# Optimization experiments

Measured on AMD Instinct MI355X. Metric: run time of the kernel, lower is better.

Reference implementation:

```python
import jax, jax.numpy as jnp
import numpy as np

N_INP = 128
N_HID = 512
N_OUT = 256
N_HEADS = 64
N_SM = 4
EPS_GN = 1e-5
TINY = 1e-14


def setup_inputs() -> dict:
    key = jax.random.key(0)
    ks = jax.random.split(key, 8)
    s = 0.05  # small init scale keeps softplus/softmax in a sane range
    f32 = jnp.float32
    return {
        "x": jax.random.normal(ks[0], (N_INP, N_INP), f32),
        "last_out_sm": jax.random.uniform(ks[1], (N_OUT, N_HEADS), f32),
        # grouped-conv weights, stored per-head with conv singleton dims squeezed
        "qw": jax.random.normal(ks[2], (N_HEADS, N_INP), f32) * s,            # Conv2d q
        "w1": jax.random.normal(ks[3], (N_HEADS, N_HID, N_INP), f32) * s,     # Conv1d l1
        "gn1_g": jnp.ones((N_HEADS, N_HID), f32),                             # GroupNorm ln_l1
        "gn1_b": jnp.zeros((N_HEADS, N_HID), f32),
        "w2": jax.random.normal(ks[4], (N_SM, N_HEADS, N_OUT, N_HID), f32) * s,  # Conv1d l2_n
        "gn2_g": jnp.ones((N_SM, N_HEADS, N_OUT), f32),                       # GroupNorm ln_l2_n
        "gn2_b": jnp.zeros((N_SM, N_HEADS, N_OUT), f32),
        "ws": jax.random.normal(ks[5], (N_HEADS, N_OUT, N_OUT), f32) * s,     # Conv1d scalar
        "woo": jax.random.normal(ks[6], (N_HEADS, 2 * N_OUT), f32) * s,       # Conv1d on_off
    }


def _group_norm(z, g, b):
    # normalize over the last (per-head channel) axis, biased variance, then affine
    mu = z.mean(-1, keepdims=True)
    var = z.var(-1, keepdims=True)
    return (z - mu) * jax.lax.rsqrt(var + EPS_GN) * g + b


def reference(x, last_out_sm, qw, w1, gn1_g, gn1_b, w2, gn2_g, gn2_b, ws, woo):
    n_out = last_out_sm.shape[0]
    # q: grouped Conv2d with kernel (1, n_inp) on replicated x -> per-head x @ qw_h
    sub = jnp.einsum("rc,hc->hr", x, qw)                     # (H, n_inp)
    # l1 (grouped 1x1 conv == per-head matmul) + GroupNorm(n_heads groups) + softplus
    h1 = jax.nn.softplus(_group_norm(jnp.einsum("hoi,hi->ho", w1, sub), gn1_g, gn1_b))  # (H, n_hid)
    # l2_n branches: per-head matmul + GroupNorm + softmax over n_out, summed over n_sm
    z = _group_norm(jnp.einsum("shoi,hi->sho", w2, h1), gn2_g, gn2_b)  # (S, H, n_out)
    out_sm = jax.nn.softmax(z, axis=-1).sum(0).T             # (n_out, H)
    # scalar branch: grouped 1x1 conv applied to ones -> row-sum of per-head weight
    scalar = ws.sum(-1).T                                    # (n_out, H)
    # on_off gate: per-head dot of [prod(last_out_sm, dim1), out_sm[:, h]] with woo_h
    last_prod = jnp.prod(last_out_sm, axis=1)                # (n_out,)
    gate_logit = woo[:, :n_out] @ last_prod + jnp.einsum("ho,oh->h", woo[:, n_out:], out_sm)
    on_off = jax.nn.sigmoid(gate_logit)                      # (H,)
    on_off_out_sm = on_off[None, :] * out_sm                 # (n_out, H)
    out_scaled = on_off_out_sm * scalar
    out_scaled = jnp.where(jnp.abs(out_scaled) <= TINY, TINY, out_scaled)
    return (jnp.clip(on_off_out_sm, TINY, None), out_scaled)
```

## Files before the change

kernel.cpp:

```cpp
#include <hip/hip_runtime.h>
#include <math.h>

#define N_INP 128
#define N_HID 512
#define N_OUT 256
#define N_HEADS 64
#define N_SM 4
#define EPS_GN 1e-5f
#define TINY 1e-14f

__device__ __forceinline__ float wave_sum(float v) {
#pragma unroll
  for (int off = 32; off; off >>= 1) v += __shfl_down(v, off);
  return v;
}
__device__ __forceinline__ float wave_max(float v) {
#pragma unroll
  for (int off = 32; off; off >>= 1) v = fmaxf(v, __shfl_down(v, off));
  return v;
}

__device__ __forceinline__ float block_sum(float v, float* red) {
  int wave = threadIdx.x >> 6, lane = threadIdx.x & 63;
  int nw = blockDim.x >> 6;
  v = wave_sum(v);
  __syncthreads();
  if (lane == 0) red[wave] = v;
  __syncthreads();
  float s = 0.f;
  for (int i = 0; i < nw; ++i) s += red[i];
  return s;
}
__device__ __forceinline__ float block_max(float v, float* red) {
  int wave = threadIdx.x >> 6, lane = threadIdx.x & 63;
  int nw = blockDim.x >> 6;
  v = wave_max(v);
  __syncthreads();
  if (lane == 0) red[wave] = v;
  __syncthreads();
  float s = -3.4e38f;
  for (int i = 0; i < nw; ++i) s = fmaxf(s, red[i]);
  return s;
}

__global__ __launch_bounds__(512) void k_z1(
    const float* __restrict__ x, const float* __restrict__ qw,
    const float* __restrict__ w1, float* __restrict__ z1,
    float* __restrict__ osm) {
  int blk = blockIdx.x;
  int h = blk >> 2, oq = blk & 3;
  int tid = threadIdx.x, wave = tid >> 6, lane = tid & 63;
  __shared__ float sub_s[N_INP];

  if (tid < 64) osm[blk * 64 + tid] = 0.f;

  float2 qv = ((const float2*)(qw + h * N_INP))[lane];
  for (int r = wave; r < N_INP; r += 8) {
    float2 xv = ((const float2*)(x + r * N_INP))[lane];
    float p = wave_sum(xv.x * qv.x + xv.y * qv.y);
    if (lane == 0) sub_s[r] = p;
  }
  __syncthreads();

  float2 sv = ((const float2*)sub_s)[lane];
  const float* w1h = w1 + ((size_t)h * N_HID + (size_t)oq * 128) * N_INP;
  for (int k = 0; k < 16; ++k) {
    int o = wave * 16 + k;
    float2 wv = ((const float2*)(w1h + (size_t)o * N_INP))[lane];
    float p = wave_sum(wv.x * sv.x + wv.y * sv.y);
    if (lane == 0) z1[h * N_HID + oq * 128 + o] = p;
  }
}

__global__ __launch_bounds__(1024) void k_l2_scalar(
    const float* __restrict__ z1, const float* __restrict__ g1,
    const float* __restrict__ b1, const float* __restrict__ w2,
    const float* __restrict__ g2, const float* __restrict__ b2,
    const float* __restrict__ wsc, float* __restrict__ osm,
    float* __restrict__ scal) {
  int blk = blockIdx.x;
  int s = blk >> 6, h = blk & 63;
  int tid = threadIdx.x, wave = tid >> 6, lane = tid & 63;
  __shared__ float h1_s[N_HID];
  __shared__ float z_s[N_OUT];
  __shared__ float red[16];

  float v1 = (tid < N_HID) ? z1[h * N_HID + tid] : 0.f;
  float s1 = block_sum(v1, red);
  float ss1 = block_sum(v1 * v1, red);
  float mu1 = s1 * (1.f / N_HID);
  float var1 = ss1 * (1.f / N_HID) - mu1 * mu1;
  float r1 = rsqrtf(var1 + EPS_GN);
  if (tid < N_HID) {
    float zz = (v1 - mu1) * r1 * g1[h * N_HID + tid] + b1[h * N_HID + tid];
    h1_s[tid] = fmaxf(zz, 0.f) + log1pf(expf(-fabsf(zz)));
  }
  __syncthreads();

  float4 ha = ((const float4*)h1_s)[lane];
  float4 hb = ((const float4*)h1_s)[64 + lane];

  for (int k = 0; k < 4; ++k) {
    int o = s * 64 + wave * 4 + k;
    float4 v = ((const float4*)(wsc + ((size_t)(h * N_OUT + o)) * N_OUT))[lane];
    float p = wave_sum(v.x + v.y + v.z + v.w);
    if (lane == 0) scal[o * N_HEADS + h] = p;
  }

  const float* w2base = w2 + (size_t)blk * N_OUT * N_HID;
  for (int k = 0; k < 16; ++k) {
    int o = wave * 16 + k;
    const float4* row = (const float4*)(w2base + (size_t)o * N_HID);
    float4 wa = row[lane];
    float4 wb = row[64 + lane];
    float p = wa.x * ha.x + wa.y * ha.y + wa.z * ha.z + wa.w * ha.w +
              wb.x * hb.x + wb.y * hb.y + wb.z * hb.z + wb.w * hb.w;
    p = wave_sum(p);
    if (lane == 0) z_s[o] = p;
  }
  __syncthreads();

  float v = (tid < N_OUT) ? z_s[tid] : 0.f;
  float sz = block_sum(v, red);
  float ssz = block_sum(v * v, red);
  float mu = sz * (1.f / N_OUT);
  float var = ssz * (1.f / N_OUT) - mu * mu;
  float rs = rsqrtf(var + EPS_GN);
  float zn = (tid < N_OUT)
                 ? (v - mu) * rs * g2[(size_t)blk * N_OUT + tid] + b2[(size_t)blk * N_OUT + tid]
                 : -3.4e38f;
  float mx = block_max(zn, red);
  float e = (tid < N_OUT) ? expf(zn - mx) : 0.f;
  float es = block_sum(e, red);
  if (tid < N_OUT) atomicAdd(&osm[tid * N_HEADS + h], e / es);
}

__global__ __launch_bounds__(256) void k_gate_final(
    const float* __restrict__ last, const float* __restrict__ woo,
    const float* __restrict__ osm, const float* __restrict__ scal,
    float* __restrict__ out) {
  int h = blockIdx.x;
  int tid = threadIdx.x;
  __shared__ float red[4];

  const float4* row = (const float4*)(last + (size_t)tid * N_HEADS);
  float p = 1.f;
#pragma unroll
  for (int j = 0; j < 16; ++j) {
    float4 v = row[j];
    p *= v.x * v.y * v.z * v.w;
  }
  float o_sm = osm[tid * N_HEADS + h];
  float part = woo[h * 2 * N_OUT + tid] * p +
               woo[h * 2 * N_OUT + N_OUT + tid] * o_sm;
  float logit = block_sum(part, red);
  float oo = 1.f / (1.f + expf(-logit));

  float v0 = oo * o_sm;
  out[tid * N_HEADS + h] = fmaxf(v0, TINY);
  float v1 = v0 * scal[tid * N_HEADS + h];
  out[N_OUT * N_HEADS + tid * N_HEADS + h] = (fabsf(v1) <= TINY) ? TINY : v1;
}

extern "C" void kernel_launch(void* const* d_in, const int* in_sizes, int n_in,
                              void* d_out, int out_size, void* d_ws, size_t ws_size,
                              hipStream_t stream) {
  const float* x    = (const float*)d_in[0];
  const float* last = (const float*)d_in[1];
  const float* qw   = (const float*)d_in[2];
  const float* w1   = (const float*)d_in[3];
  const float* g1   = (const float*)d_in[4];
  const float* b1   = (const float*)d_in[5];
  const float* w2   = (const float*)d_in[6];
  const float* g2   = (const float*)d_in[7];
  const float* b2   = (const float*)d_in[8];
  const float* wsc  = (const float*)d_in[9];
  const float* woo  = (const float*)d_in[10];
  float* out = (float*)d_out;
  float* ws  = (float*)d_ws;

  float* z1   = ws;
  float* osm  = ws + 32768;
  float* scal = ws + 49152;

  hipLaunchKernelGGL(k_z1,        dim3(256), dim3(512),  0, stream, x, qw, w1, z1, osm);
  hipLaunchKernelGGL(k_l2_scalar, dim3(256), dim3(1024), 0, stream, z1, g1, b1, w2, g2, b2, wsc, osm, scal);
  hipLaunchKernelGGL(k_gate_final,dim3(64),  dim3(256),  0, stream, last, woo, osm, scal, out);
}
```

Measured before the change: 262.5 us.

## Fuse gate/final kernel into main kernel via last-block-per-head atomic counter

Removes the third kernel launch by having the last of the four softmax-branch blocks for each head, detected with a per-head atomic counter, compute the on/off gate and write the outputs. The counter is reset in the first kernel, and scalar and osm are read back through atomics with thread fences so the other blocks' writes are visible. This saves one launch and its dependency gap. In exchange it adds fences, atomic traffic and a serialized tail inside one block per head.

Measured after the change: 328.8 us. 1.25x slower.

```diff
diff --git a/kernel.cpp b/kernel.cpp
--- a/kernel.cpp
+++ b/kernel.cpp
@@ -46,13 +46,14 @@
 __global__ __launch_bounds__(512) void k_z1(
     const float* __restrict__ x, const float* __restrict__ qw,
     const float* __restrict__ w1, float* __restrict__ z1,
-    float* __restrict__ osm) {
+    float* __restrict__ osm, int* __restrict__ cnt) {
   int blk = blockIdx.x;
   int h = blk >> 2, oq = blk & 3;
   int tid = threadIdx.x, wave = tid >> 6, lane = tid & 63;
   __shared__ float sub_s[N_INP];
 
   if (tid < 64) osm[blk * 64 + tid] = 0.f;
+  if (oq == 0 && tid == 0) cnt[h] = 0;
 
   float2 qv = ((const float2*)(qw + h * N_INP))[lane];
   for (int r = wave; r < N_INP; r += 8) {
@@ -72,18 +73,21 @@
   }
 }
 
-__global__ __launch_bounds__(1024) void k_l2_scalar(
+__global__ __launch_bounds__(1024) void k_main(
     const float* __restrict__ z1, const float* __restrict__ g1,
     const float* __restrict__ b1, const float* __restrict__ w2,
     const float* __restrict__ g2, const float* __restrict__ b2,
-    const float* __restrict__ wsc, float* __restrict__ osm,
-    float* __restrict__ scal) {
+    const float* __restrict__ wsc, const float* __restrict__ last,
+    const float* __restrict__ woo, float* __restrict__ osm,
+    float* __restrict__ scal, int* __restrict__ cnt,
+    float* __restrict__ out) {
   int blk = blockIdx.x;
   int s = blk >> 6, h = blk & 63;
   int tid = threadIdx.x, wave = tid >> 6, lane = tid & 63;
   __shared__ float h1_s[N_HID];
   __shared__ float z_s[N_OUT];
   __shared__ float red[16];
+  __shared__ int bcast;
 
   float v1 = (tid < N_HID) ? z1[h * N_HID + tid] : 0.f;
   float s1 = block_sum(v1, red);
@@ -104,7 +108,7 @@
     int o = s * 64 + wave * 4 + k;
     float4 v = ((const float4*)(wsc + ((size_t)(h * N_OUT + o)) * N_OUT))[lane];
     float p = wave_sum(v.x + v.y + v.z + v.w);
-    if (lane == 0) scal[o * N_HEADS + h] = p;
+    if (lane == 0) atomicExch(&scal[o * N_HEADS + h], p);
   }
 
   const float* w2base = w2 + (size_t)blk * N_OUT * N_HID;
@@ -133,33 +137,36 @@
   float e = (tid < N_OUT) ? expf(zn - mx) : 0.f;
   float es = block_sum(e, red);
   if (tid < N_OUT) atomicAdd(&osm[tid * N_HEADS + h], e / es);
-}
 
-__global__ __launch_bounds__(256) void k_gate_final(
-    const float* __restrict__ last, const float* __restrict__ woo,
-    const float* __restrict__ osm, const float* __restrict__ scal,
-    float* __restrict__ out) {
-  int h = blockIdx.x;
-  int tid = threadIdx.x;
-  __shared__ float red[4];
-
-  const float4* row = (const float4*)(last + (size_t)tid * N_HEADS);
-  float p = 1.f;
+  __syncthreads();
+  __threadfence();
+  if (tid == 0) bcast = atomicAdd(&cnt[h], 1);
+  __syncthreads();
+  if (bcast == 3) {
+    __threadfence();
+    float part = 0.f, o_sm = 0.f, sc = 0.f;
+    if (tid < N_OUT) {
+      const float4* row = (const float4*)(last + (size_t)tid * N_HEADS);
+      float lp = 1.f;
 #pragma unroll
-  for (int j = 0; j < 16; ++j) {
-    float4 v = row[j];
-    p *= v.x * v.y * v.z * v.w;
+      for (int j = 0; j < 16; ++j) {
+        float4 u = row[j];
+        lp *= u.x * u.y * u.z * u.w;
+      }
+      o_sm = atomicAdd(&osm[tid * N_HEADS + h], 0.f);
+      sc   = atomicAdd(&scal[tid * N_HEADS + h], 0.f);
+      part = woo[h * 2 * N_OUT + tid] * lp +
+             woo[h * 2 * N_OUT + N_OUT + tid] * o_sm;
+    }
+    float logit = block_sum(part, red);
+    float oo = 1.f / (1.f + expf(-logit));
+    if (tid < N_OUT) {
+      float v0 = oo * o_sm;
+      out[tid * N_HEADS + h] = fmaxf(v0, TINY);
+      float vv = v0 * sc;
+      out[N_OUT * N_HEADS + tid * N_HEADS + h] = (fabsf(vv) <= TINY) ? TINY : vv;
+    }
   }
-  float o_sm = osm[tid * N_HEADS + h];
-  float part = woo[h * 2 * N_OUT + tid] * p +
-               woo[h * 2 * N_OUT + N_OUT + tid] * o_sm;
-  float logit = block_sum(part, red);
-  float oo = 1.f / (1.f + expf(-logit));
-
-  float v0 = oo * o_sm;
-  out[tid * N_HEADS + h] = fmaxf(v0, TINY);
-  float v1 = v0 * scal[tid * N_HEADS + h];
-  out[N_OUT * N_HEADS + tid * N_HEADS + h] = (fabsf(v1) <= TINY) ? TINY : v1;
 }
 
 extern "C" void kernel_launch(void* const* d_in, const int* in_sizes, int n_in,
@@ -182,8 +189,9 @@
   float* z1   = ws;
   float* osm  = ws + 32768;
   float* scal = ws + 49152;
+  int*   cnt  = (int*)(ws + 65536);
 
-  hipLaunchKernelGGL(k_z1,        dim3(256), dim3(512),  0, stream, x, qw, w1, z1, osm);
-  hipLaunchKernelGGL(k_l2_scalar, dim3(256), dim3(1024), 0, stream, z1, g1, b1, w2, g2, b2, wsc, osm, scal);
-  hipLaunchKernelGGL(k_gate_final,dim3(64),  dim3(256),  0, stream, last, woo, osm, scal, out);
+  hipLaunchKernelGGL(k_z1,   dim3(256), dim3(512),  0, stream, x, qw, w1, z1, osm, cnt);
+  hipLaunchKernelGGL(k_main, dim3(256), dim3(1024), 0, stream,
+                     z1, g1, b1, w2, g2, b2, wsc, last, woo, osm, scal, cnt, out);
 }
```
